# Kernel tuning notes

Measured on AMD Instinct MI355X. Metric: run time of the kernel, lower is better.

## Reference

```python
import jax, jax.numpy as jnp
import numpy as np
from math import comb

N_DERIV = 4          # num_derivatives
ODE_DIM = 512        # ode_dimension
K = ODE_DIM * (N_DERIV + 1)


def _build_system(n, d):
    # system_matrices_1d: A_1d = flip(pascal), Q_1d = flip(hilbert), chol(Q_1d)
    x = np.arange(n + 1)
    B = np.array([[comb(i, j) for j in range(n + 1)] for i in range(n + 1)], dtype=np.float64)
    A1 = B[::-1, ::-1]                                  # flip both axes
    Hil = 1.0 / (x[:, None] + x[None, :] + 1.0)
    Q1 = Hil[::-1, ::-1]
    L1 = np.linalg.cholesky(Q1)
    a = np.kron(np.eye(d), A1)
    q = np.kron(np.eye(d), L1)
    return jnp.asarray(a, jnp.float32), jnp.asarray(q, jnp.float32)


def _qr_r(x):
    # sqrtm_to_cholesky: upper-triangular factor from reduced QR
    return jnp.linalg.qr(x)[1]


def setup_inputs() -> dict:
    key = jax.random.key(0)
    k1, k2, k3, k4, k5 = jax.random.split(key, 5)
    a, q_sqrtm_lower = _build_system(N_DERIV, ODE_DIM)
    m0 = jax.random.normal(k1, (K,), dtype=jnp.float32)
    l0 = jnp.tril(jax.random.normal(k2, (K, K), dtype=jnp.float32) * 0.05)
    H = jax.random.normal(k3, (ODE_DIM, K), dtype=jnp.float32) * 0.1
    bias = jax.random.normal(k4, (ODE_DIM,), dtype=jnp.float32)
    dt = jax.random.uniform(k5, (1,), dtype=jnp.float32, minval=0.05, maxval=0.15)
    return {"m0": m0, "l0": l0, "H": H, "bias": bias, "dt": dt,
            "a": a, "q_sqrtm_lower": q_sqrtm_lower}


def reference(m0, l0, H, bias, dt, a, q_sqrtm_lower):
    d = H.shape[0]
    k = m0.shape[0]
    n1 = k // d                       # num_derivatives + 1
    # --- assemble_preconditioner ---
    powers = jnp.arange(n1 - 1, -1, -1, dtype=m0.dtype)
    scales = jnp.exp(jax.lax.lgamma(powers + 1.0))
    pw = powers + 0.5
    adt = jnp.abs(dt[0])
    p = jnp.tile(adt ** pw / scales, d)          # (k,)
    p_inv = jnp.tile(adt ** (-pw) * scales, d)   # (k,)
    # --- extrapolate_mean ---
    m0_p = p_inv * m0
    m_ext_p = a @ m0_p
    m_ext = p * m_ext_p
    # EK-style linearized observation residual
    m_obs = H @ m_ext - bias                     # (d,)
    # --- estimate_error ---
    l_obs_ns_e = H @ (p_inv[:, None] * q_sqrtm_lower)            # (d,k)
    l_obs_raw = _qr_r(l_obs_ns_e.T).T                            # lower (d,d)
    res_white = jax.scipy.linalg.solve_triangular(l_obs_raw.T, m_obs, lower=False)
    diffusion = jnp.sqrt(jnp.dot(res_white, res_white) / res_white.size)
    error = diffusion * jnp.sqrt(jnp.einsum('nj,nj->n', l_obs_raw, l_obs_raw))
    # --- complete_extrapolation (sum_of_sqrtm_factors) ---
    R1 = (a @ (p_inv[:, None] * l0)).T           # (k,k)
    R2 = (diffusion * q_sqrtm_lower).T           # (k,k)
    l_ext_p = _qr_r(jnp.vstack([R1, R2])).T      # lower (k,k)
    l_ext = p[:, None] * l_ext_p
    # --- final_correction ---
    l_obs_ns = H @ l_ext                         # (d,k)
    l_obs = _qr_r(l_obs_ns.T).T                  # lower (d,d)
    crosscov = l_ext @ l_obs_ns.T                # (k,d)
    gain = jax.scipy.linalg.cho_solve((l_obs, True), crosscov.T).T  # (k,d)
    m_cor = m_ext - gain @ m_obs
    l_cor = l_ext - gain @ l_obs_ns
    u = jnp.reshape(m_cor, (-1, d), order='F')[0]  # derivative-0 block
    return m_cor, l_cor, u, error, diffusion
```

## Files before the change

kernel.cpp:

```cpp
#include <hip/hip_runtime.h>
#include <math.h>

#define KDIM 2560
#define DDIM 512
#define NB 64

#define QM 2560
#define QN 512
#define PW 16
#define UW 10

#define OUT_LCOR 2560
#define OUT_U    6556160
#define OUT_ERR  6556672
#define OUT_DIFF 6557184


__global__ void k_setup(const float* dt, double* scal){
  if (threadIdx.x==0 && blockIdx.x==0){
    double adt = fabs((double)dt[0]);
    const double scales[5] = {24.0,6.0,2.0,1.0,1.0};
    for (int i=0;i<5;i++){
      double pw = (double)(4-i)+0.5;
      scal[i]   = pow(adt, pw)/scales[i];
      scal[5+i] = pow(adt,-pw)*scales[i];
    }
  }
}

__global__ void k_mext(const float* a, const float* m0, const double* scal, double* mext){
  int r = blockIdx.x*blockDim.x + threadIdx.x;
  if (r>=KDIM) return;
  int j=r/5, i=r%5;
  const float* arow = a + (size_t)r*KDIM + 5*j;
  const float* m0b  = m0 + 5*j;
  double acc=0;
  for (int l=0;l<5;l++) acc += (double)arow[l]*scal[5+l]*(double)m0b[l];
  mext[r] = scal[i]*acc;
}

__global__ void k_mobs(const float* H, const float* bias, const double* mext, double* mobs){
  __shared__ double red[256];
  int r = blockIdx.x;
  const float* Hr = H + (size_t)r*KDIM;
  double acc=0;
  for (int c=threadIdx.x;c<KDIM;c+=256) acc += (double)Hr[c]*mext[c];
  red[threadIdx.x]=acc; __syncthreads();
  for (int s=128;s>0;s>>=1){ if (threadIdx.x<s) red[threadIdx.x]+=red[threadIdx.x+s]; __syncthreads(); }
  if (threadIdx.x==0) mobs[r] = red[0] - (double)bias[r];
}

__global__ void k_A(const float* H, const float* q, const double* scal, double* A){
  int idx = blockIdx.x*blockDim.x+threadIdx.x;
  if (idx >= QN*QM) return;
  int j = idx / QM;
  int i = idx % QM;
  int bi = i/5;
  double acc=0;
  for (int t=0;t<5;t++)
    acc += (double)H[(size_t)j*QM + 5*bi+t]*scal[5+t]*(double)q[(size_t)(5*bi+t)*QM + i];
  A[idx] = acc;
}

__global__ __launch_bounds__(1024) void qr_panel(double* A, double* beta, double* vhead, int col0){
  __shared__ double vbuf[QM];
  __shared__ double red[1024];
  __shared__ double sh[2];
  int tid = threadIdx.x;
  for (int j=0;j<PW;j++){
    int c = col0 + j;
    double acc = 0;
    for (int r = c + tid; r < QM; r += 1024){
      double v = A[(size_t)c*QM + r];
      vbuf[r-c] = v;
      acc += v*v;
    }
    red[tid] = acc; __syncthreads();
    for (int s=512; s>0; s>>=1){ if (tid<s) red[tid]+=red[tid+s]; __syncthreads(); }
    if (tid==0){
      double s0 = red[0];
      double x1 = vbuf[0];
      double nrm = sqrt(s0);
      double alpha = (x1 >= 0.0) ? -nrm : nrm;
      double v1 = x1 - alpha;
      double vtv = s0 - 2.0*alpha*x1 + alpha*alpha;
      double b = (vtv > 0.0) ? 2.0/vtv : 0.0;
      vbuf[0] = v1;
      sh[0] = b;
      A[(size_t)c*QM + c] = alpha;
      beta[c] = b;
      vhead[c] = v1;
    }
    __syncthreads();
    double b = sh[0];
    int wid = tid >> 6, lane = tid & 63;
    int jj = j + 1 + wid;
    if (jj < PW && b != 0.0){
      int cc = col0 + jj;
      double d = 0;
      for (int r = c + lane; r < QM; r += 64)
        d += vbuf[r-c]*A[(size_t)cc*QM + r];
      #pragma unroll
      for (int off=32; off>0; off>>=1) d += __shfl_down(d, off);
      d = __shfl(d, 0);
      double sc = b*d;
      for (int r = c + lane; r < QM; r += 64)
        A[(size_t)cc*QM + r] -= sc*vbuf[r-c];
    }
    __syncthreads();
  }
}

__global__ __launch_bounds__(512) void qr_vtvT(const double* A, const double* beta, const double* vhead,
                                               int col0, double* Tbuf){
  __shared__ double VtV[PW][PW];
  __shared__ double T[PW][PW];
  int tid = threadIdx.x, wid = tid>>6, lane = tid&63;
  for (int p = wid; p < PW*(PW-1)/2; p += 8){
    int i=0,j=1,cnt=p;
    for (j=1;j<PW;j++){ if (cnt < j){ i = cnt; break; } cnt -= j; }
    int ci = col0+i, cj = col0+j;
    double d=0;
    for (int r = cj + lane; r < QM; r += 64){
      double vi = A[(size_t)ci*QM + r];
      double vj = (r==cj) ? vhead[cj] : A[(size_t)cj*QM + r];
      d += vi*vj;
    }
    #pragma unroll
    for (int off=32;off>0;off>>=1) d += __shfl_down(d,off);
    if (lane==0) VtV[i][j]=d;
  }
  __syncthreads();
  if (tid==0){
    for (int j=0;j<PW;j++){
      double bj = beta[col0+j];
      T[j][j] = bj;
      for (int i=0;i<j;i++){
        double z=0;
        for (int t=i;t<j;t++) z += T[i][t]*VtV[t][j];
        T[i][j] = -bj*z;
      }
    }
    for (int i=0;i<PW;i++) for (int j2=0;j2<PW;j2++)
      Tbuf[i*PW+j2] = (j2>=i)? T[i][j2] : 0.0;
  }
}

__global__ __launch_bounds__(256) void qr_update(double* A, const double* vhead,
                                                 const double* Tbuf, int col0){
  __shared__ double redu[4][PW];
  __shared__ double ysh[PW];
  __shared__ double wsh[PW];
  int tid=threadIdx.x, wid=tid>>6, lane=tid&63;
  int cc=col0+PW+blockIdx.x;
  int m=QM-col0;
  double a[UW];
  #pragma unroll
  for (int w=0;w<UW;w++){
    int lr=tid+w*256;
    a[w]=(lr<m)? A[(size_t)cc*QM+col0+lr] : 0.0;
  }
  double acc[PW];
  #pragma unroll
  for (int j=0;j<PW;j++) acc[j]=0;
  #pragma unroll
  for (int w=0;w<UW;w++){
    int lr=tid+w*256;
    if (lr<m){
      #pragma unroll
      for (int j=0;j<PW;j++){
        double vj;
        if (lr>j)       vj=A[(size_t)(col0+j)*QM+col0+lr];
        else if (lr==j) vj=vhead[col0+j];
        else            vj=0.0;
        acc[j]+=vj*a[w];
      }
    }
  }
  #pragma unroll
  for (int j=0;j<PW;j++){
    double d=acc[j];
    #pragma unroll
    for (int o=32;o>0;o>>=1) d+=__shfl_down(d,o);
    if (lane==0) redu[wid][j]=d;
  }
  __syncthreads();
  if (tid<PW){
    double y=0;
    #pragma unroll
    for (int t=0;t<4;t++) y+=redu[t][tid];
    ysh[tid]=y;
  }
  __syncthreads();
  if (tid<PW){
    double s=0;
    for (int t=0;t<=tid;t++) s+=Tbuf[t*PW+tid]*ysh[t];
    wsh[tid]=s;
  }
  __syncthreads();
  #pragma unroll
  for (int w=0;w<UW;w++){
    int lr=tid+w*256;
    if (lr<m){
      double s=0;
      #pragma unroll
      for (int j=0;j<PW;j++){
        double vj;
        if (lr>j)       vj=A[(size_t)(col0+j)*QM+col0+lr];
        else if (lr==j) vj=vhead[col0+j];
        else            vj=0.0;
        s+=vj*wsh[j];
      }
      A[(size_t)cc*QM+col0+lr]=a[w]-s;
    }
  }
}

__global__ void k_extractR(const double* A, double* Rq){
  int idx = blockIdx.x*blockDim.x+threadIdx.x;
  if (idx >= QN*QN) return;
  int r = idx/QN, c = idx%QN;
  Rq[idx] = (r<=c) ? A[(size_t)c*QM + r] : 0.0;
}

__global__ void k_colnorm(const double* Rq, double* g1d){
  int c = blockIdx.x*blockDim.x+threadIdx.x;
  if (c>=QN) return;
  double s=0;
  for (int r=0;r<=c;r++){ double v=Rq[(size_t)r*QN+c]; s+=v*v; }
  g1d[c]=s;
}

__global__ __launch_bounds__(512) void k_resw(const double* Rq, const double* mobs, const double* g1d,
                                              double* scal, float* out){
  __shared__ double b[DDIM];
  __shared__ double xs[DDIM];
  __shared__ double D[NB][NB+1];
  __shared__ double red[DDIM];
  int tid=threadIdx.x;
  b[tid]=mobs[tid];
  __syncthreads();
  for (int p=7;p>=0;p--){
    int b0=p*NB;
    for (int e=tid;e<NB*NB;e+=512){int i=e>>6,j2=e&63; D[i][j2]=Rq[(size_t)(b0+i)*DDIM+b0+j2];}
    __syncthreads();
    if (tid<64){
      double bi=b[b0+tid];
      for (int k=NB-1;k>=0;k--){
        double bk=__shfl(bi,k);
        double xk=bk/D[k][k];
        if (tid<k) bi-=D[tid][k]*xk;
        if (tid==k) bi=xk;
      }
      xs[b0+tid]=bi;
    }
    __syncthreads();
    if (tid<b0){
      double s=0;
      #pragma unroll 8
      for (int j2=0;j2<NB;j2++) s+=Rq[(size_t)tid*DDIM+b0+j2]*xs[b0+j2];
      b[tid]-=s;
    }
    __syncthreads();
  }
  red[tid]=xs[tid]*xs[tid]; __syncthreads();
  for (int s=256;s>0;s>>=1){ if (tid<s) red[tid]+=red[tid+s]; __syncthreads(); }
  double diff=sqrt(red[0]/(double)DDIM);
  if (tid==0){ scal[10]=diff; out[OUT_DIFF]=(float)diff; }
  out[OUT_ERR+tid]=(float)(diff*sqrt(fmax(g1d[tid],0.0)));
}

__global__ void k_X(const float* a, const float* l0, const double* scal, float* X){
  int idx=blockIdx.x*blockDim.x+threadIdx.x;
  if (idx>=KDIM*KDIM) return;
  int r=idx/KDIM, c=idx%KDIM;
  int j=r/5;
  const float* arow = a + (size_t)r*KDIM + 5*j;
  double acc=0;
  for (int l=0;l<5;l++)
    acc += (double)arow[l]*scal[5+l]*(double)l0[(size_t)(5*j+l)*KDIM+c];
  X[idx]=(float)acc;
}

template<typename TA,int ATR,typename TB,int BTR,int MODE>
__global__ __launch_bounds__(256) void gemm64(const TA* __restrict__ A,int lda,
                                              const TB* __restrict__ B,int ldb,
                                              void* __restrict__ Cv,int ldc,
                                              int K,int kmode){
  __shared__ double As[16][65];
  __shared__ double Bs[16][65];
  int tid=threadIdx.x, tx=tid&15, ty=tid>>4;
  int n0=blockIdx.x*64, m0=blockIdx.y*64;
  int ks=0, ke=K;
  if (kmode==1) ks=n0;
  else if (kmode==2) ke=min(K,n0+64);
  double acc[4][4]={};
  for (int k0=ks;k0<ke;k0+=16){
    if (ATR){
      for (int e=tid;e<16*64;e+=256){int k=e>>6,mm=e&63; As[k][mm]=(double)A[(size_t)(k0+k)*lda+m0+mm];}
    } else {
      for (int e=tid;e<64*16;e+=256){int mm=e>>4,k=e&15; As[k][mm]=(double)A[(size_t)(m0+mm)*lda+k0+k];}
    }
    if (BTR){
      for (int e=tid;e<64*16;e+=256){int nn=e>>4,k=e&15; Bs[k][nn]=(double)B[(size_t)(n0+nn)*ldb+k0+k];}
    } else {
      for (int e=tid;e<16*64;e+=256){int k=e>>6,nn=e&63; Bs[k][nn]=(double)B[(size_t)(k0+k)*ldb+n0+nn];}
    }
    __syncthreads();
    #pragma unroll
    for (int t=0;t<16;t++){
      double av[4],bv[4];
      #pragma unroll
      for (int i=0;i<4;i++){av[i]=As[t][ty+16*i];bv[i]=Bs[t][tx+16*i];}
      #pragma unroll
      for (int i=0;i<4;i++)
        #pragma unroll
        for (int j=0;j<4;j++) acc[i][j]+=av[i]*bv[j];
    }
    __syncthreads();
  }
  #pragma unroll
  for (int i=0;i<4;i++){
    #pragma unroll
    for (int j=0;j<4;j++){
      size_t idx=(size_t)(m0+ty+16*i)*ldc+n0+tx+16*j;
      if (MODE==0) ((double*)Cv)[idx]=acc[i][j];
      else if (MODE==1) ((double*)Cv)[idx]-=acc[i][j];
      else ((float*)Cv)[idx]=(float)acc[i][j];
    }
  }
}

__global__ __launch_bounds__(256) void syrk_lower(const float* __restrict__ X, double* __restrict__ G, int n){
  int S0=blockIdx.x*64, R0=blockIdx.y*64;
  if (S0>R0) return;
  __shared__ double As[16][65];
  __shared__ double Bs[16][65];
  int tid=threadIdx.x, tx=tid&15, ty=tid>>4;
  int kend=min(n, S0+80);
  double acc[4][4]={};
  for (int k0=0;k0<kend;k0+=16){
    for (int e=tid;e<64*16;e+=256){int mm=e>>4,k=e&15; As[k][mm]=(double)X[(size_t)(R0+mm)*n+k0+k];}
    for (int e=tid;e<64*16;e+=256){int nn=e>>4,k=e&15; Bs[k][nn]=(double)X[(size_t)(S0+nn)*n+k0+k];}
    __syncthreads();
    #pragma unroll
    for (int t=0;t<16;t++){
      double av[4],bv[4];
      #pragma unroll
      for (int i=0;i<4;i++){av[i]=As[t][ty+16*i];bv[i]=Bs[t][tx+16*i];}
      #pragma unroll
      for (int i=0;i<4;i++)
        #pragma unroll
        for (int j=0;j<4;j++) acc[i][j]+=av[i]*bv[j];
    }
    __syncthreads();
  }
  #pragma unroll
  for (int i=0;i<4;i++)
    #pragma unroll
    for (int j=0;j<4;j++)
      G[(size_t)(R0+ty+16*i)*n+S0+tx+16*j]=acc[i][j];
}

__global__ void k_addqqt(const float* q, const double* scal, double* G2){
  int idx=blockIdx.x*blockDim.x+threadIdx.x;
  if (idx>=DDIM*15) return;
  int j=idx/15, t=idx%15;
  int i=0; while (t >= i+1){ t-=i+1; i++; }
  int jj=t;
  double acc=0;
  for (int k=0;k<5;k++) acc += (double)q[(size_t)i*KDIM+k]*(double)q[(size_t)jj*KDIM+k];
  double dd=scal[10]*scal[10];
  G2[(size_t)(5*j+i)*KDIM + 5*j+jj] += dd*acc;
}

__global__ __launch_bounds__(256) void chol_diag(double* A, int n, int k0){
  __shared__ double P[NB][NB+1];
  int tid=threadIdx.x;
  for (int e=tid;e<NB*NB;e+=256){int r=e>>6,c=e&63;P[r][c]=A[(size_t)(k0+r)*n+k0+c];}
  int tx=tid&15, ty=tid>>4;
  __syncthreads();
  for (int j=0;j<NB;j++){
    double pj=P[j][j];
    __syncthreads();
    double rpj=1.0/sqrt(fmax(pj,1e-280));
    if (tid>j && tid<NB) P[tid][j]*=rpj;
    if (tid==j) P[j][j]=sqrt(fmax(pj,1e-280));
    __syncthreads();
    #pragma unroll
    for (int a2=0;a2<4;a2++){
      int r=ty+16*a2;
      double lrj=P[r][j];
      #pragma unroll
      for (int b2=0;b2<4;b2++){
        int c=tx+16*b2;
        if (r>j && c>j && c<=r) P[r][c]-=lrj*P[c][j];
      }
    }
    __syncthreads();
  }
  for (int e=tid;e<NB*NB;e+=256){int r=e>>6,c=e&63;A[(size_t)(k0+r)*n+k0+c]=P[r][c];}
}

__global__ __launch_bounds__(256) void chol_trsm(double* A,int n,int k0){
  __shared__ double Ls[NB][NB+1];
  __shared__ double St[NB][NB+1];
  __shared__ double rec[NB];
  int tid=threadIdx.x;
  for (int e=tid;e<NB*NB;e+=256){int r=e>>6,c=e&63;Ls[r][c]=A[(size_t)(k0+r)*n+k0+c];}
  __syncthreads();
  if (tid<NB) rec[tid]=1.0/Ls[tid][tid];
  int base=k0+NB+blockIdx.x*256;
  int myrow=base+tid;
  int mychunk=tid>>6, lrow=tid&63;
  double ar[NB];
  for (int ch=0;ch<4;ch++){
    int r0=base+ch*64;
    for (int e=tid;e<NB*NB;e+=256){
      int r=e>>6,c=e&63;
      if (r0+r<n) St[r][c]=A[(size_t)(r0+r)*n+k0+c];
    }
    __syncthreads();
    if (mychunk==ch && myrow<n){
      #pragma unroll
      for (int c=0;c<NB;c++) ar[c]=St[lrow][c];
    }
    __syncthreads();
  }
  if (myrow<n){
    #pragma unroll
    for (int j=0;j<NB;j++){
      double s=ar[j];
      #pragma unroll
      for (int t=0;t<j;t++) s-=ar[t]*Ls[j][t];
      ar[j]=s*rec[j];
    }
  }
  for (int ch=0;ch<4;ch++){
    int r0=base+ch*64;
    if (mychunk==ch && myrow<n){
      #pragma unroll
      for (int c=0;c<NB;c++) St[lrow][c]=ar[c];
    }
    __syncthreads();
    for (int e=tid;e<NB*NB;e+=256){
      int r=e>>6,c=e&63;
      if (r0+r<n) A[(size_t)(r0+r)*n+k0+c]=St[r][c];
    }
    __syncthreads();
  }
}

__global__ __launch_bounds__(256) void chol_syrk(double* A,int n,int k0){
  int ts0=k0+NB;
  int S0=ts0+blockIdx.x*64, R0=ts0+blockIdx.y*64;
  if (S0>R0) return;
  __shared__ double As[16][65];
  __shared__ double Bs[16][65];
  int tid=threadIdx.x, tx=tid&15, ty=tid>>4;
  double acc[4][4]={};
  for (int k0i=0;k0i<NB;k0i+=16){
    for (int e=tid;e<64*16;e+=256){int mm=e>>4,k=e&15; As[k][mm]=A[(size_t)(R0+mm)*n+k0+k0i+k];}
    for (int e=tid;e<64*16;e+=256){int nn=e>>4,k=e&15; Bs[k][nn]=A[(size_t)(S0+nn)*n+k0+k0i+k];}
    __syncthreads();
    #pragma unroll
    for (int t=0;t<16;t++){
      double av[4],bv[4];
      #pragma unroll
      for (int i=0;i<4;i++){av[i]=As[t][ty+16*i];bv[i]=Bs[t][tx+16*i];}
      #pragma unroll
      for (int i=0;i<4;i++)
        #pragma unroll
        for (int j=0;j<4;j++) acc[i][j]+=av[i]*bv[j];
    }
    __syncthreads();
  }
  #pragma unroll
  for (int i=0;i<4;i++)
    #pragma unroll
    for (int j=0;j<4;j++)
      A[(size_t)(R0+ty+16*i)*n+S0+tx+16*j]-=acc[i][j];
}

static void chol_blocked(double* A, int n, hipStream_t stream){
  for (int k0=0;k0<n;k0+=NB){
    chol_diag<<<1,256,0,stream>>>(A,n,k0);
    int m = n-k0-NB;
    if (m>0){
      chol_trsm<<<(m+255)/256,256,0,stream>>>(A,n,k0);
      chol_syrk<<<dim3(m/64,m/64),256,0,stream>>>(A,n,k0);
    }
  }
}

__global__ void k_extract(const double* G2, const double* scal, float* lext){
  int idx=blockIdx.x*blockDim.x+threadIdx.x;
  if (idx>=KDIM*KDIM) return;
  int r=idx/KDIM, c=idx%KDIM;
  double v = (c<=r)? scal[r%5]*G2[idx] : 0.0;
  lext[idx]=(float)v;
}

__global__ __launch_bounds__(256) void trsm_fwd(const double* __restrict__ L,int n,int b0,
                                                double* __restrict__ Z,int ldz){
  __shared__ double Ls[NB][NB+1];
  __shared__ double rec[NB];
  int lin=threadIdx.x;
  for (int e=lin;e<NB*NB;e+=256){int r=e>>6,c=e&63;Ls[r][c]=L[(size_t)(b0+r)*n+b0+c];}
  __syncthreads();
  if (lin<NB) rec[lin]=1.0/Ls[lin][lin];
  __syncthreads();
  int col=blockIdx.x*256+lin;
  double z[NB];
  #pragma unroll
  for (int r=0;r<NB;r++) z[r]=Z[(size_t)(b0+r)*ldz+col];
  #pragma unroll
  for (int r=0;r<NB;r++){
    double s=z[r];
    #pragma unroll
    for (int t=0;t<r;t++) s-=Ls[r][t]*z[t];
    z[r]=s*rec[r];
  }
  #pragma unroll
  for (int r=0;r<NB;r++) Z[(size_t)(b0+r)*ldz+col]=z[r];
}

__global__ __launch_bounds__(256) void trsm_bwd(const double* __restrict__ L,int n,int b0,
                                                double* __restrict__ Z,int ldz){
  __shared__ double Ls[NB][NB+1];
  __shared__ double rec[NB];
  int lin=threadIdx.x;
  for (int e=lin;e<NB*NB;e+=256){int r=e>>6,c=e&63;Ls[r][c]=L[(size_t)(b0+r)*n+b0+c];}
  __syncthreads();
  if (lin<NB) rec[lin]=1.0/Ls[lin][lin];
  __syncthreads();
  int col=blockIdx.x*256+lin;
  double z[NB];
  #pragma unroll
  for (int r=0;r<NB;r++) z[r]=Z[(size_t)(b0+r)*ldz+col];
  #pragma unroll
  for (int ri=NB-1;ri>=0;ri--){
    double s=z[ri];
    #pragma unroll
    for (int t=ri+1;t<NB;t++) s-=Ls[t][ri]*z[t];
    z[ri]=s*rec[ri];
  }
  #pragma unroll
  for (int r=0;r<NB;r++) Z[(size_t)(b0+r)*ldz+col]=z[r];
}

__global__ void k_mcor(const double* Z, const double* mobs, const double* mext, float* out){
  __shared__ double mo[DDIM];
  for (int s=threadIdx.x;s<DDIM;s+=256) mo[s]=mobs[s];
  __syncthreads();
  int r=blockIdx.x*256+threadIdx.x;
  if (r>=KDIM) return;
  double acc=0;
  for (int s=0;s<DDIM;s++) acc += Z[(size_t)s*KDIM+r]*mo[s];
  double mc = mext[r]-acc;
  out[r]=(float)mc;
  if (r%5==0) out[OUT_U + r/5]=(float)mc;
}

__global__ __launch_bounds__(256) void k_lcor(const double* __restrict__ Z, const float* __restrict__ lobs,
                                              const float* __restrict__ lext, float* __restrict__ out){
  __shared__ double As[16][65];
  __shared__ double Bs[16][65];
  int tid=threadIdx.x, tx=tid&15, ty=tid>>4;
  int n0=blockIdx.x*64, m0=blockIdx.y*64;
  double acc[4][4]={};
  for (int k0=0;k0<DDIM;k0+=16){
    for (int e=tid;e<16*64;e+=256){int k=e>>6,mm=e&63; As[k][mm]=Z[(size_t)(k0+k)*KDIM+m0+mm];}
    for (int e=tid;e<16*64;e+=256){int k=e>>6,nn=e&63; Bs[k][nn]=(double)lobs[(size_t)(k0+k)*KDIM+n0+nn];}
    __syncthreads();
    #pragma unroll
    for (int t=0;t<16;t++){
      double av[4],bv[4];
      #pragma unroll
      for (int i=0;i<4;i++){av[i]=As[t][ty+16*i];bv[i]=Bs[t][tx+16*i];}
      #pragma unroll
      for (int i=0;i<4;i++)
        #pragma unroll
        for (int j=0;j<4;j++) acc[i][j]+=av[i]*bv[j];
    }
    __syncthreads();
  }
  #pragma unroll
  for (int i=0;i<4;i++)
    #pragma unroll
    for (int j=0;j<4;j++){
      size_t idx=(size_t)(m0+ty+16*i)*KDIM+n0+tx+16*j;
      out[OUT_LCOR+idx]=(float)((double)lext[idx]-acc[i][j]);
    }
}

extern "C" void kernel_launch(void* const* d_in, const int* in_sizes, int n_in,
                              void* d_out, int out_size, void* d_ws, size_t ws_size,
                              hipStream_t stream) {
  const float* m0  = (const float*)d_in[0];
  const float* l0  = (const float*)d_in[1];
  const float* H   = (const float*)d_in[2];
  const float* bias= (const float*)d_in[3];
  const float* dt  = (const float*)d_in[4];
  const float* a   = (const float*)d_in[5];
  const float* q   = (const float*)d_in[6];
  float* out = (float*)d_out;

  char* w=(char*)d_ws;
  auto alloc=[&](size_t bytes)->char*{ char* p=w; w += ((bytes+255)/256)*256; return p; };
  double* scal =(double*)alloc(16*8);
  double* mext =(double*)alloc((size_t)KDIM*8);
  double* mobs =(double*)alloc((size_t)DDIM*8);
  double* g1d  =(double*)alloc((size_t)DDIM*8);
  double* betaA=(double*)alloc((size_t)QN*8);
  double* vheadA=(double*)alloc((size_t)QN*8);
  double* Tbuf =(double*)alloc((size_t)PW*PW*8);
  double* Aq   =(double*)alloc((size_t)QM*QN*8);
  double* Rq   =(double*)alloc((size_t)QN*QN*8);
  double* S    =(double*)alloc((size_t)DDIM*DDIM*8);
  double* G2   =(double*)alloc((size_t)KDIM*KDIM*8);
  float*  LOBS =(float*) alloc((size_t)DDIM*KDIM*4);
  float*  X    =(float*) alloc((size_t)KDIM*KDIM*4);
  double* Z    = G2;
  float*  LEXT = X;

  k_setup<<<1,1,0,stream>>>(dt, scal);
  k_mext<<<(KDIM+255)/256,256,0,stream>>>(a, m0, scal, mext);
  k_mobs<<<DDIM,256,0,stream>>>(H, bias, mext, mobs);

  k_A<<<(QN*QM+255)/256,256,0,stream>>>(H, q, scal, Aq);
  for (int p=0;p<QN/PW;p++){
    int col0=p*PW;
    qr_panel<<<1,1024,0,stream>>>(Aq, betaA, vheadA, col0);
    int ntr = QN - col0 - PW;
    if (ntr>0){
      qr_vtvT<<<1,512,0,stream>>>(Aq,betaA,vheadA,col0,Tbuf);
      qr_update<<<ntr,256,0,stream>>>(Aq, vheadA, Tbuf, col0);
    }
  }
  k_extractR<<<(QN*QN+255)/256,256,0,stream>>>(Aq, Rq);
  k_colnorm<<<(QN+255)/256,256,0,stream>>>(Rq, g1d);
  k_resw<<<1,512,0,stream>>>(Rq, mobs, g1d, scal, out);

  k_X<<<(KDIM*KDIM+255)/256,256,0,stream>>>(a, l0, scal, X);
  syrk_lower<<<dim3(KDIM/64,KDIM/64),256,0,stream>>>(X, G2, KDIM);
  k_addqqt<<<(DDIM*15+255)/256,256,0,stream>>>(q, scal, G2);
  chol_blocked(G2, KDIM, stream);
  k_extract<<<(KDIM*KDIM+255)/256,256,0,stream>>>(G2, scal, LEXT);

  gemm64<float,0,float,0,2><<<dim3(KDIM/64,DDIM/64),256,0,stream>>>(H,KDIM, LEXT,KDIM, LOBS,KDIM, KDIM, 1);
  gemm64<float,0,float,1,0><<<dim3(DDIM/64,DDIM/64),256,0,stream>>>(LOBS,KDIM, LOBS,KDIM, S,DDIM, KDIM, 0);
  chol_blocked(S, DDIM, stream);
  gemm64<float,0,float,1,0><<<dim3(KDIM/64,DDIM/64),256,0,stream>>>(LOBS,KDIM, LEXT,KDIM, Z,KDIM, KDIM, 2);
  for (int b=0;b<DDIM;b+=NB){
    trsm_fwd<<<KDIM/256,256,0,stream>>>(S, DDIM, b, Z, KDIM);
    int m = DDIM-b-NB;
    if (m>0)
      gemm64<double,0,double,0,1><<<dim3(KDIM/64,m/64),256,0,stream>>>(
        S+(size_t)(b+NB)*DDIM+b, DDIM, Z+(size_t)b*KDIM, KDIM,
        Z+(size_t)(b+NB)*KDIM, KDIM, NB, 0);
  }
  for (int b=DDIM-NB;b>=0;b-=NB){
    trsm_bwd<<<KDIM/256,256,0,stream>>>(S, DDIM, b, Z, KDIM);
    if (b>0)
      gemm64<double,1,double,0,1><<<dim3(KDIM/64,b/64),256,0,stream>>>(
        S+(size_t)b*DDIM, DDIM, Z+(size_t)b*KDIM, KDIM,
        Z, KDIM, NB, 0);
  }

  k_mcor<<<(KDIM+255)/256,256,0,stream>>>(Z, mobs, mext, out);
  k_lcor<<<dim3(KDIM/64,KDIM/64),256,0,stream>>>(Z, LOBS, LEXT, out);
}
```

Before: 18.19 ms.

## Fuse setup kernels, merge QR T-build into panel, invert L_obs for gain solve

```diff
diff --git a/kernel.cpp b/kernel.cpp
--- a/kernel.cpp
+++ b/kernel.cpp
@@ -16,57 +16,69 @@
 #define OUT_DIFF 6557184
 
 
-__global__ void k_setup(const float* dt, double* scal){
-  if (threadIdx.x==0 && blockIdx.x==0){
-    double adt = fabs((double)dt[0]);
-    const double scales[5] = {24.0,6.0,2.0,1.0,1.0};
-    for (int i=0;i<5;i++){
-      double pw = (double)(4-i)+0.5;
-      scal[i]   = pow(adt, pw)/scales[i];
-      scal[5+i] = pow(adt,-pw)*scales[i];
-    }
-  }
-}
-
-__global__ void k_mext(const float* a, const float* m0, const double* scal, double* mext){
-  int r = blockIdx.x*blockDim.x + threadIdx.x;
-  if (r>=KDIM) return;
-  int j=r/5, i=r%5;
-  const float* arow = a + (size_t)r*KDIM + 5*j;
-  const float* m0b  = m0 + 5*j;
+__device__ __forceinline__ void get_pats(const float* dt, double* pp, double* pv){
+  double adt = fabs((double)dt[0]);
+  const double scales[5] = {24.0,6.0,2.0,1.0,1.0};
+  #pragma unroll
+  for (int i=0;i<5;i++){
+    double pw = (double)(4-i)+0.5;
+    pp[i] = pow(adt, pw)/scales[i];
+    pv[i] = pow(adt,-pw)*scales[i];
+  }
+}
+
+__global__ __launch_bounds__(256) void k_mext_mobs(const float* a, const float* m0, const float* H,
+                                                   const float* bias, const float* dt,
+                                                   double* mext, double* mobs){
+  __shared__ double me[KDIM];
+  __shared__ double red[256];
+  double pp[5], pv[5];
+  get_pats(dt, pp, pv);
+  int tid=threadIdx.x;
+  for (int r=tid; r<KDIM; r+=256){
+    int j=r/5, i=r%5;
+    const float* arow = a + (size_t)r*KDIM + 5*j;
+    const float* m0b  = m0 + 5*j;
+    double acc=0;
+    #pragma unroll
+    for (int l=0;l<5;l++) acc += (double)arow[l]*pv[l]*(double)m0b[l];
+    me[r] = pp[i]*acc;
+  }
+  __syncthreads();
+  if (blockIdx.x==0) for (int r=tid;r<KDIM;r+=256) mext[r]=me[r];
+  int b = blockIdx.x;
+  const float* Hr = H + (size_t)b*KDIM;
   double acc=0;
-  for (int l=0;l<5;l++) acc += (double)arow[l]*scal[5+l]*(double)m0b[l];
-  mext[r] = scal[i]*acc;
-}
-
-__global__ void k_mobs(const float* H, const float* bias, const double* mext, double* mobs){
-  __shared__ double red[256];
-  int r = blockIdx.x;
-  const float* Hr = H + (size_t)r*KDIM;
-  double acc=0;
-  for (int c=threadIdx.x;c<KDIM;c+=256) acc += (double)Hr[c]*mext[c];
-  red[threadIdx.x]=acc; __syncthreads();
-  for (int s=128;s>0;s>>=1){ if (threadIdx.x<s) red[threadIdx.x]+=red[threadIdx.x+s]; __syncthreads(); }
-  if (threadIdx.x==0) mobs[r] = red[0] - (double)bias[r];
-}
-
-__global__ void k_A(const float* H, const float* q, const double* scal, double* A){
+  for (int c=tid;c<KDIM;c+=256) acc += (double)Hr[c]*me[c];
+  red[tid]=acc; __syncthreads();
+  for (int s=128;s>0;s>>=1){ if (tid<s) red[tid]+=red[tid+s]; __syncthreads(); }
+  if (tid==0) mobs[b] = red[0] - (double)bias[b];
+}
+
+__global__ void k_A(const float* H, const float* q, const float* dt, double* A){
   int idx = blockIdx.x*blockDim.x+threadIdx.x;
   if (idx >= QN*QM) return;
+  double pp[5], pv[5];
+  get_pats(dt, pp, pv);
   int j = idx / QM;
   int i = idx % QM;
   int bi = i/5;
   double acc=0;
+  #pragma unroll
   for (int t=0;t<5;t++)
-    acc += (double)H[(size_t)j*QM + 5*bi+t]*scal[5+t]*(double)q[(size_t)(5*bi+t)*QM + i];
+    acc += (double)H[(size_t)j*QM + 5*bi+t]*pv[t]*(double)q[(size_t)(5*bi+t)*QM + i];
   A[idx] = acc;
 }
 
-__global__ __launch_bounds__(1024) void qr_panel(double* A, double* beta, double* vhead, int col0){
+__global__ __launch_bounds__(1024) void qr_panel(double* A, double* vhead, int col0, double* Tbuf){
   __shared__ double vbuf[QM];
   __shared__ double red[1024];
   __shared__ double sh[2];
+  __shared__ double VtVs[PW][PW];
+  __shared__ double betas_s[PW];
+  __shared__ double Tsh[PW][PW];
   int tid = threadIdx.x;
+  int wid = tid >> 6, lane = tid & 63;
   for (int j=0;j<PW;j++){
     int c = col0 + j;
     double acc = 0;
@@ -88,12 +100,11 @@
       vbuf[0] = v1;
       sh[0] = b;
       A[(size_t)c*QM + c] = alpha;
-      beta[c] = b;
+      betas_s[j] = b;
       vhead[c] = v1;
     }
     __syncthreads();
     double b = sh[0];
-    int wid = tid >> 6, lane = tid & 63;
     int jj = j + 1 + wid;
     if (jj < PW && b != 0.0){
       int cc = col0 + jj;
@@ -107,42 +118,32 @@
       for (int r = c + lane; r < QM; r += 64)
         A[(size_t)cc*QM + r] -= sc*vbuf[r-c];
     }
-    __syncthreads();
-  }
-}
-
-__global__ __launch_bounds__(512) void qr_vtvT(const double* A, const double* beta, const double* vhead,
-                                               int col0, double* Tbuf){
-  __shared__ double VtV[PW][PW];
-  __shared__ double T[PW][PW];
-  int tid = threadIdx.x, wid = tid>>6, lane = tid&63;
-  for (int p = wid; p < PW*(PW-1)/2; p += 8){
-    int i=0,j=1,cnt=p;
-    for (j=1;j<PW;j++){ if (cnt < j){ i = cnt; break; } cnt -= j; }
-    int ci = col0+i, cj = col0+j;
-    double d=0;
-    for (int r = cj + lane; r < QM; r += 64){
-      double vi = A[(size_t)ci*QM + r];
-      double vj = (r==cj) ? vhead[cj] : A[(size_t)cj*QM + r];
-      d += vi*vj;
-    }
-    #pragma unroll
-    for (int off=32;off>0;off>>=1) d += __shfl_down(d,off);
-    if (lane==0) VtV[i][j]=d;
-  }
-  __syncthreads();
+    if (wid < j){
+      int i = wid;
+      double d = 0;
+      for (int r = c + lane; r < QM; r += 64)
+        d += vbuf[r-c]*A[(size_t)(col0+i)*QM + r];
+      #pragma unroll
+      for (int off=32; off>0; off>>=1) d += __shfl_down(d, off);
+      if (lane==0) VtVs[i][j] = d;
+    }
+    __syncthreads();
+  }
   if (tid==0){
     for (int j=0;j<PW;j++){
-      double bj = beta[col0+j];
-      T[j][j] = bj;
+      double bj = betas_s[j];
+      Tsh[j][j] = bj;
       for (int i=0;i<j;i++){
         double z=0;
-        for (int t=i;t<j;t++) z += T[i][t]*VtV[t][j];
-        T[i][j] = -bj*z;
+        for (int t=i;t<j;t++) z += Tsh[i][t]*VtVs[t][j];
+        Tsh[i][j] = -bj*z;
       }
     }
-    for (int i=0;i<PW;i++) for (int j2=0;j2<PW;j2++)
-      Tbuf[i*PW+j2] = (j2>=i)? T[i][j2] : 0.0;
+  }
+  __syncthreads();
+  for (int e=tid;e<PW*PW;e+=1024){
+    int i=e/PW, j2=e%PW;
+    Tbuf[e] = (j2>=i)? Tsh[i][j2] : 0.0;
   }
 }
 
@@ -216,33 +217,24 @@
   }
 }
 
-__global__ void k_extractR(const double* A, double* Rq){
-  int idx = blockIdx.x*blockDim.x+threadIdx.x;
-  if (idx >= QN*QN) return;
-  int r = idx/QN, c = idx%QN;
-  Rq[idx] = (r<=c) ? A[(size_t)c*QM + r] : 0.0;
-}
-
-__global__ void k_colnorm(const double* Rq, double* g1d){
-  int c = blockIdx.x*blockDim.x+threadIdx.x;
-  if (c>=QN) return;
-  double s=0;
-  for (int r=0;r<=c;r++){ double v=Rq[(size_t)r*QN+c]; s+=v*v; }
-  g1d[c]=s;
-}
-
-__global__ __launch_bounds__(512) void k_resw(const double* Rq, const double* mobs, const double* g1d,
-                                              double* scal, float* out){
+__global__ __launch_bounds__(512) void k_rpost(const double* Aq, const double* mobs,
+                                               double* scal, float* out){
   __shared__ double b[DDIM];
   __shared__ double xs[DDIM];
   __shared__ double D[NB][NB+1];
   __shared__ double red[DDIM];
+  __shared__ double g1sh[DDIM];
   int tid=threadIdx.x;
+  {
+    double s=0;
+    for (int r=0;r<=tid;r++){ double v=Aq[(size_t)tid*QM + r]; s+=v*v; }
+    g1sh[tid]=s;
+  }
   b[tid]=mobs[tid];
   __syncthreads();
   for (int p=7;p>=0;p--){
     int b0=p*NB;
-    for (int e=tid;e<NB*NB;e+=512){int i=e>>6,j2=e&63; D[i][j2]=Rq[(size_t)(b0+i)*DDIM+b0+j2];}
+    for (int e=tid;e<NB*NB;e+=512){ int i=e&63, j2=e>>6; D[i][j2]=Aq[(size_t)(b0+j2)*QM + b0+i]; }
     __syncthreads();
     if (tid<64){
       double bi=b[b0+tid];
@@ -258,7 +250,7 @@
     if (tid<b0){
       double s=0;
       #pragma unroll 8
-      for (int j2=0;j2<NB;j2++) s+=Rq[(size_t)tid*DDIM+b0+j2]*xs[b0+j2];
+      for (int j2=0;j2<NB;j2++) s+=Aq[(size_t)(b0+j2)*QM + tid]*xs[b0+j2];
       b[tid]-=s;
     }
     __syncthreads();
@@ -267,18 +259,21 @@
   for (int s=256;s>0;s>>=1){ if (tid<s) red[tid]+=red[tid+s]; __syncthreads(); }
   double diff=sqrt(red[0]/(double)DDIM);
   if (tid==0){ scal[10]=diff; out[OUT_DIFF]=(float)diff; }
-  out[OUT_ERR+tid]=(float)(diff*sqrt(fmax(g1d[tid],0.0)));
-}
-
-__global__ void k_X(const float* a, const float* l0, const double* scal, float* X){
+  out[OUT_ERR+tid]=(float)(diff*sqrt(fmax(g1sh[tid],0.0)));
+}
+
+__global__ void k_X(const float* a, const float* l0, const float* dt, float* X){
   int idx=blockIdx.x*blockDim.x+threadIdx.x;
   if (idx>=KDIM*KDIM) return;
+  double pp[5], pv[5];
+  get_pats(dt, pp, pv);
   int r=idx/KDIM, c=idx%KDIM;
   int j=r/5;
   const float* arow = a + (size_t)r*KDIM + 5*j;
   double acc=0;
+  #pragma unroll
   for (int l=0;l<5;l++)
-    acc += (double)arow[l]*scal[5+l]*(double)l0[(size_t)(5*j+l)*KDIM+c];
+    acc += (double)arow[l]*pv[l]*(double)l0[(size_t)(5*j+l)*KDIM+c];
   X[idx]=(float)acc;
 }
 
@@ -294,6 +289,8 @@
   int ks=0, ke=K;
   if (kmode==1) ks=n0;
   else if (kmode==2) ke=min(K,n0+64);
+  else if (kmode==3) ke=min(K,m0+64);
+  else if (kmode==4) ks=m0;
   double acc[4][4]={};
   for (int k0=ks;k0<ke;k0+=16){
     if (ATR){
@@ -331,7 +328,9 @@
   }
 }
 
-__global__ __launch_bounds__(256) void syrk_lower(const float* __restrict__ X, double* __restrict__ G, int n){
+__global__ __launch_bounds__(256) void syrk_lower(const float* __restrict__ X, const float* __restrict__ q,
+                                                  const double* __restrict__ scal,
+                                                  double* __restrict__ G, int n){
   int S0=blockIdx.x*64, R0=blockIdx.y*64;
   if (S0>R0) return;
   __shared__ double As[16][65];
@@ -355,23 +354,21 @@
     }
     __syncthreads();
   }
+  double dd = scal[10]*scal[10];
   #pragma unroll
   for (int i=0;i<4;i++)
     #pragma unroll
-    for (int j=0;j<4;j++)
-      G[(size_t)(R0+ty+16*i)*n+S0+tx+16*j]=acc[i][j];
-}
-
-__global__ void k_addqqt(const float* q, const double* scal, double* G2){
-  int idx=blockIdx.x*blockDim.x+threadIdx.x;
-  if (idx>=DDIM*15) return;
-  int j=idx/15, t=idx%15;
-  int i=0; while (t >= i+1){ t-=i+1; i++; }
-  int jj=t;
-  double acc=0;
-  for (int k=0;k<5;k++) acc += (double)q[(size_t)i*KDIM+k]*(double)q[(size_t)jj*KDIM+k];
-  double dd=scal[10]*scal[10];
-  G2[(size_t)(5*j+i)*KDIM + 5*j+jj] += dd*acc;
+    for (int j=0;j<4;j++){
+      int r=R0+ty+16*i, c=S0+tx+16*j;
+      double v=acc[i][j];
+      if (c<=r && (r/5)==(c/5)){
+        double qq=0;
+        #pragma unroll
+        for (int k=0;k<5;k++) qq += (double)q[(size_t)(r%5)*KDIM+k]*(double)q[(size_t)(c%5)*KDIM+k];
+        v += dd*qq;
+      }
+      G[(size_t)r*n+c]=v;
+    }
 }
 
 __global__ __launch_bounds__(256) void chol_diag(double* A, int n, int k0){
@@ -451,12 +448,13 @@
   }
 }
 
-__global__ __launch_bounds__(256) void chol_syrk(double* A,int n,int k0){
+__global__ __launch_bounds__(256) void chol_syrk_fd(double* A,int n,int k0){
   int ts0=k0+NB;
   int S0=ts0+blockIdx.x*64, R0=ts0+blockIdx.y*64;
   if (S0>R0) return;
   __shared__ double As[16][65];
   __shared__ double Bs[16][65];
+  __shared__ double P[NB][NB+1];
   int tid=threadIdx.x, tx=tid&15, ty=tid>>4;
   double acc[4][4]={};
   for (int k0i=0;k0i<NB;k0i+=16){
@@ -475,78 +473,125 @@
     }
     __syncthreads();
   }
+  if (!(blockIdx.x==0 && blockIdx.y==0)){
+    #pragma unroll
+    for (int i=0;i<4;i++)
+      #pragma unroll
+      for (int j=0;j<4;j++)
+        A[(size_t)(R0+ty+16*i)*n+S0+tx+16*j]-=acc[i][j];
+    return;
+  }
   #pragma unroll
   for (int i=0;i<4;i++)
     #pragma unroll
     for (int j=0;j<4;j++)
-      A[(size_t)(R0+ty+16*i)*n+S0+tx+16*j]-=acc[i][j];
-}
-
-static void chol_blocked(double* A, int n, hipStream_t stream){
-  for (int k0=0;k0<n;k0+=NB){
-    chol_diag<<<1,256,0,stream>>>(A,n,k0);
-    int m = n-k0-NB;
-    if (m>0){
-      chol_trsm<<<(m+255)/256,256,0,stream>>>(A,n,k0);
-      chol_syrk<<<dim3(m/64,m/64),256,0,stream>>>(A,n,k0);
-    }
-  }
-}
-
-__global__ void k_extract(const double* G2, const double* scal, float* lext){
+      P[ty+16*i][tx+16*j] = A[(size_t)(R0+ty+16*i)*n+S0+tx+16*j] - acc[i][j];
+  __syncthreads();
+  for (int j=0;j<NB;j++){
+    double pj=P[j][j];
+    __syncthreads();
+    double rpj=1.0/sqrt(fmax(pj,1e-280));
+    if (tid>j && tid<NB) P[tid][j]*=rpj;
+    if (tid==j) P[j][j]=sqrt(fmax(pj,1e-280));
+    __syncthreads();
+    #pragma unroll
+    for (int a2=0;a2<4;a2++){
+      int r=ty+16*a2;
+      double lrj=P[r][j];
+      #pragma unroll
+      for (int b2=0;b2<4;b2++){
+        int c=tx+16*b2;
+        if (r>j && c>j && c<=r) P[r][c]-=lrj*P[c][j];
+      }
+    }
+    __syncthreads();
+  }
+  for (int e=tid;e<NB*NB;e+=256){int r=e>>6,c=e&63;A[(size_t)(ts0+r)*n+ts0+c]=P[r][c];}
+}
+
+__global__ void k_extract(const double* G2, const float* dt, float* lext){
   int idx=blockIdx.x*blockDim.x+threadIdx.x;
   if (idx>=KDIM*KDIM) return;
+  double pp[5], pv[5];
+  get_pats(dt, pp, pv);
   int r=idx/KDIM, c=idx%KDIM;
-  double v = (c<=r)? scal[r%5]*G2[idx] : 0.0;
+  double v = (c<=r)? pp[r%5]*G2[idx] : 0.0;
   lext[idx]=(float)v;
 }
 
-__global__ __launch_bounds__(256) void trsm_fwd(const double* __restrict__ L,int n,int b0,
-                                                double* __restrict__ Z,int ldz){
+__global__ __launch_bounds__(256) void trinv_diag(const double* S, double* Linv){
   __shared__ double Ls[NB][NB+1];
-  __shared__ double rec[NB];
-  int lin=threadIdx.x;
-  for (int e=lin;e<NB*NB;e+=256){int r=e>>6,c=e&63;Ls[r][c]=L[(size_t)(b0+r)*n+b0+c];}
-  __syncthreads();
-  if (lin<NB) rec[lin]=1.0/Ls[lin][lin];
-  __syncthreads();
-  int col=blockIdx.x*256+lin;
-  double z[NB];
-  #pragma unroll
-  for (int r=0;r<NB;r++) z[r]=Z[(size_t)(b0+r)*ldz+col];
-  #pragma unroll
-  for (int r=0;r<NB;r++){
-    double s=z[r];
-    #pragma unroll
-    for (int t=0;t<r;t++) s-=Ls[r][t]*z[t];
-    z[r]=s*rec[r];
-  }
-  #pragma unroll
-  for (int r=0;r<NB;r++) Z[(size_t)(b0+r)*ldz+col]=z[r];
-}
-
-__global__ __launch_bounds__(256) void trsm_bwd(const double* __restrict__ L,int n,int b0,
-                                                double* __restrict__ Z,int ldz){
-  __shared__ double Ls[NB][NB+1];
-  __shared__ double rec[NB];
-  int lin=threadIdx.x;
-  for (int e=lin;e<NB*NB;e+=256){int r=e>>6,c=e&63;Ls[r][c]=L[(size_t)(b0+r)*n+b0+c];}
-  __syncthreads();
-  if (lin<NB) rec[lin]=1.0/Ls[lin][lin];
-  __syncthreads();
-  int col=blockIdx.x*256+lin;
-  double z[NB];
-  #pragma unroll
-  for (int r=0;r<NB;r++) z[r]=Z[(size_t)(b0+r)*ldz+col];
-  #pragma unroll
-  for (int ri=NB-1;ri>=0;ri--){
-    double s=z[ri];
-    #pragma unroll
-    for (int t=ri+1;t<NB;t++) s-=Ls[t][ri]*z[t];
-    z[ri]=s*rec[ri];
-  }
-  #pragma unroll
-  for (int r=0;r<NB;r++) Z[(size_t)(b0+r)*ldz+col]=z[r];
+  __shared__ double Ti[NB][NB+1];
+  int jb=blockIdx.x, tid=threadIdx.x;
+  for (int e=tid; e<DDIM*NB; e+=256){
+    int r=e/NB, c=e%NB;
+    Linv[(size_t)r*DDIM + jb*NB + c]=0.0;
+  }
+  for (int e=tid;e<NB*NB;e+=256){int r=e>>6,c=e&63; Ls[r][c]=S[(size_t)(jb*NB+r)*DDIM + jb*NB+c];}
+  __syncthreads();
+  if (tid<NB){
+    int c=tid;
+    for (int r=c;r<NB;r++){
+      double s=(r==c)?1.0:0.0;
+      for (int t=c;t<r;t++) s-=Ls[r][t]*Ti[t][c];
+      Ti[r][c]=s/Ls[r][r];
+    }
+    for (int r=0;r<c;r++) Ti[r][c]=0.0;
+  }
+  __syncthreads();
+  for (int e=tid;e<NB*NB;e+=256){int r=e>>6,c=e&63; Linv[(size_t)(jb*NB+r)*DDIM + jb*NB+c]=Ti[r][c];}
+}
+
+__global__ __launch_bounds__(256) void trinv_step(const double* S, double* Linv, int d){
+  __shared__ double As[16][65];
+  __shared__ double Bs[16][65];
+  __shared__ double Ps[NB][NB+1];
+  int jb=blockIdx.x, ib=jb+d;
+  int tid=threadIdx.x, tx=tid&15, ty=tid>>4;
+  double acc[4][4]={};
+  int kstart=jb*NB, kend=ib*NB;
+  for (int k0=kstart;k0<kend;k0+=16){
+    for (int e=tid;e<64*16;e+=256){int mm=e>>4,k=e&15; As[k][mm]=S[(size_t)(ib*NB+mm)*DDIM + k0+k];}
+    for (int e=tid;e<16*64;e+=256){int k=e>>6,nn=e&63; Bs[k][nn]=Linv[(size_t)(k0+k)*DDIM + jb*NB+nn];}
+    __syncthreads();
+    #pragma unroll
+    for (int t=0;t<16;t++){
+      double av[4],bv[4];
+      #pragma unroll
+      for (int i=0;i<4;i++){av[i]=As[t][ty+16*i];bv[i]=Bs[t][tx+16*i];}
+      #pragma unroll
+      for (int i=0;i<4;i++)
+        #pragma unroll
+        for (int j=0;j<4;j++) acc[i][j]+=av[i]*bv[j];
+    }
+    __syncthreads();
+  }
+  #pragma unroll
+  for (int i=0;i<4;i++)
+    #pragma unroll
+    for (int j=0;j<4;j++) Ps[ty+16*i][tx+16*j]=acc[i][j];
+  double o[4][4]={};
+  __syncthreads();
+  for (int k0=0;k0<NB;k0+=16){
+    for (int e=tid;e<64*16;e+=256){int mm=e>>4,k=e&15; As[k][mm]=Linv[(size_t)(ib*NB+mm)*DDIM + ib*NB+k0+k];}
+    __syncthreads();
+    #pragma unroll
+    for (int t=0;t<16;t++){
+      double av[4],bv[4];
+      #pragma unroll
+      for (int i=0;i<4;i++){av[i]=As[t][ty+16*i];bv[i]=Ps[k0+t][tx+16*i];}
+      #pragma unroll
+      for (int i=0;i<4;i++)
+        #pragma unroll
+        for (int j=0;j<4;j++) o[i][j]+=av[i]*bv[j];
+    }
+    __syncthreads();
+  }
+  #pragma unroll
+  for (int i=0;i<4;i++)
+    #pragma unroll
+    for (int j=0;j<4;j++)
+      Linv[(size_t)(ib*NB+ty+16*i)*DDIM + jb*NB+tx+16*j] = -o[i][j];
 }
 
 __global__ void k_mcor(const double* Z, const double* mobs, const double* mext, float* out){
@@ -608,65 +653,57 @@
 
   char* w=(char*)d_ws;
   auto alloc=[&](size_t bytes)->char*{ char* p=w; w += ((bytes+255)/256)*256; return p; };
-  double* scal =(double*)alloc(16*8);
-  double* mext =(double*)alloc((size_t)KDIM*8);
-  double* mobs =(double*)alloc((size_t)DDIM*8);
-  double* g1d  =(double*)alloc((size_t)DDIM*8);
-  double* betaA=(double*)alloc((size_t)QN*8);
+  double* scal  =(double*)alloc(16*8);
+  double* mext  =(double*)alloc((size_t)KDIM*8);
+  double* mobs  =(double*)alloc((size_t)DDIM*8);
   double* vheadA=(double*)alloc((size_t)QN*8);
-  double* Tbuf =(double*)alloc((size_t)PW*PW*8);
-  double* Aq   =(double*)alloc((size_t)QM*QN*8);
-  double* Rq   =(double*)alloc((size_t)QN*QN*8);
-  double* S    =(double*)alloc((size_t)DDIM*DDIM*8);
-  double* G2   =(double*)alloc((size_t)KDIM*KDIM*8);
-  float*  LOBS =(float*) alloc((size_t)DDIM*KDIM*4);
-  float*  X    =(float*) alloc((size_t)KDIM*KDIM*4);
-  double* Z    = G2;
-  float*  LEXT = X;
-
-  k_setup<<<1,1,0,stream>>>(dt, scal);
-  k_mext<<<(KDIM+255)/256,256,0,stream>>>(a, m0, scal, mext);
-  k_mobs<<<DDIM,256,0,stream>>>(H, bias, mext, mobs);
-
-  k_A<<<(QN*QM+255)/256,256,0,stream>>>(H, q, scal, Aq);
+  double* Tbuf  =(double*)alloc((size_t)PW*PW*8);
+  double* Aq    =(double*)alloc((size_t)QM*QN*8);
+  double* S     =(double*)alloc((size_t)DDIM*DDIM*8);
+  double* G2    =(double*)alloc((size_t)KDIM*KDIM*8);
+  float*  LOBS  =(float*) alloc((size_t)DDIM*KDIM*4);
+  float*  X     =(float*) alloc((size_t)KDIM*KDIM*4);
+  float*  LEXT  = X;
+  double* Linv  = G2;
+  double* C2    = Linv + (size_t)DDIM*DDIM;
+  double* Y     = C2   + (size_t)DDIM*KDIM;
+  double* Z     = Y    + (size_t)DDIM*KDIM;
+
+  k_mext_mobs<<<DDIM,256,0,stream>>>(a, m0, H, bias, dt, mext, mobs);
+
+  k_A<<<(QN*QM+255)/256,256,0,stream>>>(H, q, dt, Aq);
   for (int p=0;p<QN/PW;p++){
     int col0=p*PW;
-    qr_panel<<<1,1024,0,stream>>>(Aq, betaA, vheadA, col0);
+    qr_panel<<<1,1024,0,stream>>>(Aq, vheadA, col0, Tbuf);
     int ntr = QN - col0 - PW;
-    if (ntr>0){
-      qr_vtvT<<<1,512,0,stream>>>(Aq,betaA,vheadA,col0,Tbuf);
-      qr_update<<<ntr,256,0,stream>>>(Aq, vheadA, Tbuf, col0);
-    }
-  }
-  k_extractR<<<(QN*QN+255)/256,256,0,stream>>>(Aq, Rq);
-  k_colnorm<<<(QN+255)/256,256,0,stream>>>(Rq, g1d);
-  k_resw<<<1,512,0,stream>>>(Rq, mobs, g1d, scal, out);
-
-  k_X<<<(KDIM*KDIM+255)/256,256,0,stream>>>(a, l0, scal, X);
-  syrk_lower<<<dim3(KDIM/64,KDIM/64),256,0,stream>>>(X, G2, KDIM);
-  k_addqqt<<<(DDIM*15+255)/256,256,0,stream>>>(q, scal, G2);
-  chol_blocked(G2, KDIM, stream);
-  k_extract<<<(KDIM*KDIM+255)/256,256,0,stream>>>(G2, scal, LEXT);
+    if (ntr>0) qr_update<<<ntr,256,0,stream>>>(Aq, vheadA, Tbuf, col0);
+  }
+  k_rpost<<<1,512,0,stream>>>(Aq, mobs, scal, out);
+
+  k_X<<<(KDIM*KDIM+255)/256,256,0,stream>>>(a, l0, dt, X);
+  syrk_lower<<<dim3(KDIM/64,KDIM/64),256,0,stream>>>(X, q, scal, G2, KDIM);
+  chol_diag<<<1,256,0,stream>>>(G2, KDIM, 0);
+  for (int k0=0;k0+NB<KDIM;k0+=NB){
+    int m = KDIM-k0-NB;
+    chol_trsm<<<(m+255)/256,256,0,stream>>>(G2, KDIM, k0);
+    chol_syrk_fd<<<dim3(m/64,m/64),256,0,stream>>>(G2, KDIM, k0);
+  }
+  k_extract<<<(KDIM*KDIM+255)/256,256,0,stream>>>(G2, dt, LEXT);
 
   gemm64<float,0,float,0,2><<<dim3(KDIM/64,DDIM/64),256,0,stream>>>(H,KDIM, LEXT,KDIM, LOBS,KDIM, KDIM, 1);
   gemm64<float,0,float,1,0><<<dim3(DDIM/64,DDIM/64),256,0,stream>>>(LOBS,KDIM, LOBS,KDIM, S,DDIM, KDIM, 0);
-  chol_blocked(S, DDIM, stream);
-  gemm64<float,0,float,1,0><<<dim3(KDIM/64,DDIM/64),256,0,stream>>>(LOBS,KDIM, LEXT,KDIM, Z,KDIM, KDIM, 2);
-  for (int b=0;b<DDIM;b+=NB){
-    trsm_fwd<<<KDIM/256,256,0,stream>>>(S, DDIM, b, Z, KDIM);
-    int m = DDIM-b-NB;
-    if (m>0)
-      gemm64<double,0,double,0,1><<<dim3(KDIM/64,m/64),256,0,stream>>>(
-        S+(size_t)(b+NB)*DDIM+b, DDIM, Z+(size_t)b*KDIM, KDIM,
-        Z+(size_t)(b+NB)*KDIM, KDIM, NB, 0);
-  }
-  for (int b=DDIM-NB;b>=0;b-=NB){
-    trsm_bwd<<<KDIM/256,256,0,stream>>>(S, DDIM, b, Z, KDIM);
-    if (b>0)
-      gemm64<double,1,double,0,1><<<dim3(KDIM/64,b/64),256,0,stream>>>(
-        S+(size_t)b*DDIM, DDIM, Z+(size_t)b*KDIM, KDIM,
-        Z, KDIM, NB, 0);
-  }
+  chol_diag<<<1,256,0,stream>>>(S, DDIM, 0);
+  for (int k0=0;k0+NB<DDIM;k0+=NB){
+    int m = DDIM-k0-NB;
+    chol_trsm<<<(m+255)/256,256,0,stream>>>(S, DDIM, k0);
+    chol_syrk_fd<<<dim3(m/64,m/64),256,0,stream>>>(S, DDIM, k0);
+  }
+  trinv_diag<<<8,256,0,stream>>>(S, Linv);
+  for (int d=1;d<8;d++)
+    trinv_step<<<8-d,256,0,stream>>>(S, Linv, d);
+  gemm64<float,0,float,1,0><<<dim3(KDIM/64,DDIM/64),256,0,stream>>>(LOBS,KDIM, LEXT,KDIM, C2,KDIM, KDIM, 2);
+  gemm64<double,0,double,0,0><<<dim3(KDIM/64,DDIM/64),256,0,stream>>>(Linv,DDIM, C2,KDIM, Y,KDIM, DDIM, 3);
+  gemm64<double,1,double,0,0><<<dim3(KDIM/64,DDIM/64),256,0,stream>>>(Linv,DDIM, Y,KDIM, Z,KDIM, DDIM, 4);
 
   k_mcor<<<(KDIM+255)/256,256,0,stream>>>(Z, mobs, mext, out);
   k_lcor<<<dim3(KDIM/64,KDIM/64),256,0,stream>>>(Z, LOBS, LEXT, out);
```

After: 17.14 ms. 5.7% less time.
